# Optimization experiments

Hardware: AMD Instinct MI355X
Metric: run time of the kernel (lower is better)

## Reference

```python
import jax, jax.numpy as jnp
import numpy as np

N = 50000
E = 600000
D = 128
EPS = 1e-5  # nn.LayerNorm default eps


def gcn_conv(x, W, b, src, dst):
    # PyG GCNConv with add_self_loops=True, edge_weight=None (all ones),
    # symmetric normalization D^-1/2 (A+I) D^-1/2.
    h = x @ W                                        # [N, D]
    deg = jnp.zeros((N,), h.dtype).at[dst].add(1.0) + 1.0  # +1 for self loop
    dinv = jax.lax.rsqrt(deg)                        # deg >= 1, safe
    norm = dinv[src] * dinv[dst]                     # [E]
    msg = h[src] * norm[:, None]                     # [E, D] gather
    agg = jax.ops.segment_sum(msg, dst, num_segments=N)
    agg = agg + h * (dinv * dinv)[:, None]           # self-loop term
    return agg + b


def layer_norm(x, g, b):
    mu = jnp.mean(x, axis=-1, keepdims=True)
    var = jnp.mean(jnp.square(x - mu), axis=-1, keepdims=True)
    return (x - mu) * jax.lax.rsqrt(var + EPS) * g + b


def setup_inputs() -> dict:
    key = jax.random.key(0)
    ks = jax.random.split(key, 6)
    x = jax.random.normal(ks[0], (N, D), dtype=jnp.float32)
    edge_index = jax.random.randint(ks[1], (2, E), 0, N, dtype=jnp.int64)
    s = 1.0 / np.sqrt(D)
    W1 = jax.random.uniform(ks[2], (D, D), jnp.float32, -s, s)
    W2 = jax.random.uniform(ks[3], (D, D), jnp.float32, -s, s)
    b1 = jnp.zeros((D,), jnp.float32)
    b2 = jnp.zeros((D,), jnp.float32)
    ln1_g = jnp.ones((D,), jnp.float32)
    ln1_b = jnp.zeros((D,), jnp.float32)
    ln2_g = jnp.ones((D,), jnp.float32)
    ln2_b = jnp.zeros((D,), jnp.float32)
    return {"x": x, "edge_index": edge_index, "W1": W1, "b1": b1,
            "ln1_g": ln1_g, "ln1_b": ln1_b, "W2": W2, "b2": b2,
            "ln2_g": ln2_g, "ln2_b": ln2_b}


def reference(x, edge_index, W1, b1, ln1_g, ln1_b, W2, b2, ln2_g, ln2_b):
    src, dst = edge_index[0], edge_index[1]
    out = gcn_conv(x, W1, b1, src, dst)
    out = jax.nn.relu(layer_norm(out, ln1_g, ln1_b))  # dropout = identity (eval)
    out = gcn_conv(out, W2, b2, src, dst)
    out = jax.nn.relu(layer_norm(out, ln2_g, ln2_b))
    return out + x
```

## Files before the change

kernel.cpp:

```cpp
#include <hip/hip_runtime.h>
#include <hip/hip_fp16.h>

#define D 128
#define EPS 1e-5f

typedef unsigned int u32;
typedef unsigned short u16;
typedef __attribute__((ext_vector_type(8))) _Float16 half8;
typedef __attribute__((ext_vector_type(4))) float f32x4;

__device__ inline u16 f2h(float x) {
  _Float16 t = (_Float16)x;
  return __builtin_bit_cast(u16, t);
}
__device__ inline __half2 b2h2(u32 u) { return __builtin_bit_cast(__half2, u); }

__global__ __launch_bounds__(256) void k_prep(const float* __restrict__ W1,
                                              const float* __restrict__ W2,
                                              u16* __restrict__ Wt1,
                                              u16* __restrict__ Wt2,
                                              int* __restrict__ deg,
                                              int* __restrict__ counter, int n) {
  int i = blockIdx.x * 256 + threadIdx.x;
  if (i < n) deg[i] = 0;
  if (i == 0) *counter = 0;
  if (i < 2 * D * D) {
    const float* W = (i < D * D) ? W1 : W2;
    u16* Wt = (i < D * D) ? Wt1 : Wt2;
    int ii = i & (D * D - 1);
    int k = ii >> 7, c = ii & 127;
    Wt[c * D + k] = f2h(W[ii]);
  }
}

template <bool F32IN>
__device__ __forceinline__ void gemm_body(const void* __restrict__ in_,
                                          const u16* __restrict__ Wt,
                                          u16* __restrict__ out, int nrows,
                                          int blk) {
  const int tid = threadIdx.x;
  const int lane = tid & 63, wv = tid >> 6;
  const int m = lane & 15, q = lane >> 4;
  const int r0 = blk * 64 + wv * 16;
  const int rowa = min(r0 + m, nrows - 1);

  f32x4 acc[8];
#pragma unroll
  for (int ct = 0; ct < 8; ct++) acc[ct] = (f32x4)(0.0f);

#pragma unroll
  for (int kk = 0; kk < 4; kk++) {
    const int kbase = kk * 32 + q * 8;
    half8 a;
    if (F32IN) {
      const float* in = (const float*)in_;
      float4 v0 = *(const float4*)(in + (size_t)rowa * D + kbase);
      float4 v1 = *(const float4*)(in + (size_t)rowa * D + kbase + 4);
      a[0] = (_Float16)v0.x; a[1] = (_Float16)v0.y;
      a[2] = (_Float16)v0.z; a[3] = (_Float16)v0.w;
      a[4] = (_Float16)v1.x; a[5] = (_Float16)v1.y;
      a[6] = (_Float16)v1.z; a[7] = (_Float16)v1.w;
    } else {
      const u16* in = (const u16*)in_;
      a = *(const half8*)(in + (size_t)rowa * D + kbase);
    }
#pragma unroll
    for (int ct = 0; ct < 8; ct++) {
      half8 b = *(const half8*)(Wt + (ct * 16 + m) * D + kbase);
      acc[ct] = __builtin_amdgcn_mfma_f32_16x16x32_f16(a, b, acc[ct], 0, 0, 0);
    }
  }

#pragma unroll
  for (int ct = 0; ct < 8; ct++) {
#pragma unroll
    for (int rg = 0; rg < 4; rg++) {
      int rr = r0 + q * 4 + rg;
      if (rr < nrows) out[(size_t)rr * D + ct * 16 + m] = f2h(acc[ct][rg]);
    }
  }
}

__global__ __launch_bounds__(256) void k_deg_gemm1(
    const int* __restrict__ dst, int* __restrict__ deg, int* __restrict__ rank,
    int E, int DB,
    const float* __restrict__ x, const u16* __restrict__ Wt1,
    u16* __restrict__ A, int nrows) {
  if (blockIdx.x < (u32)DB) {
    int base = blockIdx.x * 1024 + threadIdx.x;
    int e0 = base, e1 = base + 256, e2 = base + 512, e3 = base + 768;
    int d0 = (e0 < E) ? dst[e0] : 0;
    int d1 = (e1 < E) ? dst[e1] : 0;
    int d2 = (e2 < E) ? dst[e2] : 0;
    int d3 = (e3 < E) ? dst[e3] : 0;
    int r0 = 0, r1 = 0, r2 = 0, r3 = 0;
    if (e0 < E) r0 = atomicAdd(&deg[d0], 1);
    if (e1 < E) r1 = atomicAdd(&deg[d1], 1);
    if (e2 < E) r2 = atomicAdd(&deg[d2], 1);
    if (e3 < E) r3 = atomicAdd(&deg[d3], 1);
    if (e0 < E) rank[e0] = r0;
    if (e1 < E) rank[e1] = r1;
    if (e2 < E) rank[e2] = r2;
    if (e3 < E) rank[e3] = r3;
  } else {
    gemm_body<true>(x, Wt1, A, nrows, blockIdx.x - DB);
  }
}

__global__ __launch_bounds__(256) void k_alloc(const int* __restrict__ deg,
                                               float* __restrict__ dinv,
                                               int4* __restrict__ meta,
                                               int* __restrict__ counter, int n) {
  int i = blockIdx.x * 256 + threadIdx.x;
  int lane = threadIdx.x & 63;
  int d = (i < n) ? deg[i] : 0;
  float dv = rsqrtf((float)d + 1.0f);
  int v = d;
#pragma unroll
  for (int o = 1; o < 64; o <<= 1) {
    int t = __shfl_up(v, o, 64);
    if (lane >= o) v += t;
  }
  int total = __shfl(v, 63, 64);
  int base = 0;
  if (lane == 0) base = atomicAdd(counter, total);
  base = __shfl(base, 0, 64);
  if (i < n) {
    int st = base + v - d;
    dinv[i] = dv;
    meta[i] = make_int4(st, d, __builtin_bit_cast(int, dv), 0);
  }
}

__global__ __launch_bounds__(256) void k_fill(
    const int* __restrict__ src, const int* __restrict__ dst,
    const int* __restrict__ rank, const int4* __restrict__ meta,
    const float* __restrict__ dinv, u32* __restrict__ csr, int E) {
  int base = blockIdx.x * 1024 + threadIdx.x;
#pragma unroll
  for (int t = 0; t < 4; t++) {
    int e = base + t * 256;
    if (e < E) {
      int s = src[e], d = dst[e];
      int4 mt = meta[d];
      float w = dinv[s] * __builtin_bit_cast(float, mt.z);
      csr[mt.x + rank[e]] = (u32)s | ((u32)f2h(w) << 16);
    }
  }
}

__device__ __forceinline__ void gather_ln_core(
    const uint4* __restrict__ hb, const int4* __restrict__ meta,
    const u32* __restrict__ csr, const float* __restrict__ b,
    const float* __restrict__ g, const float* __restrict__ bln,
    int row, int n, int sl, float out[8]) {
  const bool valid = row < n;
  const int rc = valid ? row : 0;
  int4 mt = meta[rc];
  int beg = mt.x;
  int cnt = valid ? mt.y : 0;
  float dv = __builtin_bit_cast(float, mt.z);
  __half2 sn2 = __float2half2_rn(dv * dv);

  uint4 su = hb[(size_t)rc * 16 + sl];
  __half2 acc0 = __hmul2(b2h2(su.x), sn2);
  __half2 acc1 = __hmul2(b2h2(su.y), sn2);
  __half2 acc2 = __hmul2(b2h2(su.z), sn2);
  __half2 acc3 = __hmul2(b2h2(su.w), sn2);

  int cm = max(cnt, __shfl_xor(cnt, 16, 64));
  cm = max(cm, __shfl_xor(cm, 32, 64));

  for (int j0 = 0; j0 < cm; j0 += 16) {
    u32 e = 0u;
    if (sl < cnt - j0) e = csr[beg + j0 + sl];
    int mm = min(cm - j0, 16);
    for (int j = 0; j < mm; j += 4) {
      u32 e0 = __shfl(e, j, 16),     e1 = __shfl(e, j + 1, 16);
      u32 e2 = __shfl(e, j + 2, 16), e3 = __shfl(e, j + 3, 16);
      uint4 v0 = hb[(size_t)(e0 & 0xffffu) * 16 + sl];
      uint4 v1 = hb[(size_t)(e1 & 0xffffu) * 16 + sl];
      uint4 v2 = hb[(size_t)(e2 & 0xffffu) * 16 + sl];
      uint4 v3 = hb[(size_t)(e3 & 0xffffu) * 16 + sl];
      __half2 w0 = b2h2((e0 >> 16) | (e0 & 0xffff0000u));
      __half2 w1 = b2h2((e1 >> 16) | (e1 & 0xffff0000u));
      __half2 w2 = b2h2((e2 >> 16) | (e2 & 0xffff0000u));
      __half2 w3 = b2h2((e3 >> 16) | (e3 & 0xffff0000u));
      acc0 = __hfma2(b2h2(v0.x), w0, acc0);
      acc1 = __hfma2(b2h2(v0.y), w0, acc1);
      acc2 = __hfma2(b2h2(v0.z), w0, acc2);
      acc3 = __hfma2(b2h2(v0.w), w0, acc3);
      acc0 = __hfma2(b2h2(v1.x), w1, acc0);
      acc1 = __hfma2(b2h2(v1.y), w1, acc1);
      acc2 = __hfma2(b2h2(v1.z), w1, acc2);
      acc3 = __hfma2(b2h2(v1.w), w1, acc3);
      acc0 = __hfma2(b2h2(v2.x), w2, acc0);
      acc1 = __hfma2(b2h2(v2.y), w2, acc1);
      acc2 = __hfma2(b2h2(v2.z), w2, acc2);
      acc3 = __hfma2(b2h2(v2.w), w2, acc3);
      acc0 = __hfma2(b2h2(v3.x), w3, acc0);
      acc1 = __hfma2(b2h2(v3.y), w3, acc1);
      acc2 = __hfma2(b2h2(v3.z), w3, acc2);
      acc3 = __hfma2(b2h2(v3.w), w3, acc3);
    }
  }

  float2 f0 = __half22float2(acc0);
  float2 f1 = __half22float2(acc1);
  float2 f2 = __half22float2(acc2);
  float2 f3 = __half22float2(acc3);
  int d0 = sl * 8;
  float4 bb0 = *(const float4*)(b + d0);
  float4 bb1 = *(const float4*)(b + d0 + 4);
  float a0 = f0.x + bb0.x, a1 = f0.y + bb0.y;
  float a2 = f1.x + bb0.z, a3 = f1.y + bb0.w;
  float a4 = f2.x + bb1.x, a5 = f2.y + bb1.y;
  float a6 = f3.x + bb1.z, a7 = f3.y + bb1.w;

  float sum = ((a0 + a1) + (a2 + a3)) + ((a4 + a5) + (a6 + a7));
#pragma unroll
  for (int o = 8; o >= 1; o >>= 1) sum += __shfl_xor(sum, o, 16);
  float mu = sum * (1.0f / 128.0f);
  float e0 = a0 - mu, e1 = a1 - mu, e2 = a2 - mu, e3 = a3 - mu;
  float e4 = a4 - mu, e5 = a5 - mu, e6 = a6 - mu, e7 = a7 - mu;
  float vs = ((e0 * e0 + e1 * e1) + (e2 * e2 + e3 * e3)) +
             ((e4 * e4 + e5 * e5) + (e6 * e6 + e7 * e7));
#pragma unroll
  for (int o = 8; o >= 1; o >>= 1) vs += __shfl_xor(vs, o, 16);
  float inv = rsqrtf(vs * (1.0f / 128.0f) + EPS);

  float4 gg0 = *(const float4*)(g + d0);
  float4 gg1 = *(const float4*)(g + d0 + 4);
  float4 bl0 = *(const float4*)(bln + d0);
  float4 bl1 = *(const float4*)(bln + d0 + 4);
  out[0] = fmaxf(e0 * inv * gg0.x + bl0.x, 0.0f);
  out[1] = fmaxf(e1 * inv * gg0.y + bl0.y, 0.0f);
  out[2] = fmaxf(e2 * inv * gg0.z + bl0.z, 0.0f);
  out[3] = fmaxf(e3 * inv * gg0.w + bl0.w, 0.0f);
  out[4] = fmaxf(e4 * inv * gg1.x + bl1.x, 0.0f);
  out[5] = fmaxf(e5 * inv * gg1.y + bl1.y, 0.0f);
  out[6] = fmaxf(e6 * inv * gg1.z + bl1.z, 0.0f);
  out[7] = fmaxf(e7 * inv * gg1.w + bl1.w, 0.0f);
}

__global__ __launch_bounds__(256) void k_mid(
    const uint4* __restrict__ hb, const int4* __restrict__ meta,
    const u32* __restrict__ csr,
    const float* __restrict__ b, const float* __restrict__ g,
    const float* __restrict__ bln,
    const u16* __restrict__ Wt2, u16* __restrict__ outB, int n) {
  __shared__ alignas(16) u16 sY[64 * 136];
  const int tid = threadIdx.x;
  const int sl = tid & 15;
  const int row0 = blockIdx.x * 64;

  for (int p = 0; p < 4; p++) {
    int lr = p * 16 + (tid >> 4);
    int row = row0 + lr;
    float o[8];
    gather_ln_core(hb, meta, csr, b, g, bln, row, n, sl, o);
    uint4 pk;
    pk.x = ((u32)f2h(o[1]) << 16) | (u32)f2h(o[0]);
    pk.y = ((u32)f2h(o[3]) << 16) | (u32)f2h(o[2]);
    pk.z = ((u32)f2h(o[5]) << 16) | (u32)f2h(o[4]);
    pk.w = ((u32)f2h(o[7]) << 16) | (u32)f2h(o[6]);
    *(uint4*)(sY + lr * 136 + sl * 8) = pk;
  }
  __syncthreads();

  const int lane = tid & 63, wv = tid >> 6;
  const int m = lane & 15, q = lane >> 4;
  f32x4 acc[8];
#pragma unroll
  for (int ct = 0; ct < 8; ct++) acc[ct] = (f32x4)(0.0f);
  const u16* ap = sY + (wv * 16 + m) * 136 + q * 8;
#pragma unroll
  for (int kk = 0; kk < 4; kk++) {
    half8 a = *(const half8*)(ap + kk * 32);
#pragma unroll
    for (int ct = 0; ct < 8; ct++) {
      half8 bfr = *(const half8*)(Wt2 + (ct * 16 + m) * D + kk * 32 + q * 8);
      acc[ct] = __builtin_amdgcn_mfma_f32_16x16x32_f16(a, bfr, acc[ct], 0, 0, 0);
    }
  }
#pragma unroll
  for (int ct = 0; ct < 8; ct++) {
#pragma unroll
    for (int rg = 0; rg < 4; rg++) {
      int rr = row0 + wv * 16 + q * 4 + rg;
      if (rr < n) outB[(size_t)rr * D + ct * 16 + m] = f2h(acc[ct][rg]);
    }
  }
}

__global__ __launch_bounds__(256) void k_gather2(
    const uint4* __restrict__ hb, const int4* __restrict__ meta,
    const u32* __restrict__ csr,
    const float* __restrict__ b, const float* __restrict__ g,
    const float* __restrict__ bln, const float* __restrict__ resid,
    float* __restrict__ outf, int n) {
  const int tid = threadIdx.x;
  const int sl = tid & 15;
  const int row = blockIdx.x * 16 + (tid >> 4);
  float o[8];
  gather_ln_core(hb, meta, csr, b, g, bln, row, n, sl, o);
  if (row >= n) return;
  size_t base = (size_t)row * D + sl * 8;
  float4 r0 = *(const float4*)(resid + base);
  float4 r1 = *(const float4*)(resid + base + 4);
  *(float4*)(outf + base) =
      make_float4(o[0] + r0.x, o[1] + r0.y, o[2] + r0.z, o[3] + r0.w);
  *(float4*)(outf + base + 4) =
      make_float4(o[4] + r1.x, o[5] + r1.y, o[6] + r1.z, o[7] + r1.w);
}

extern "C" void kernel_launch(void* const* d_in, const int* in_sizes, int n_in,
                              void* d_out, int out_size, void* d_ws, size_t ws_size,
                              hipStream_t stream) {
  const float* x    = (const float*)d_in[0];
  const int*   ei   = (const int*)d_in[1];
  const float* W1   = (const float*)d_in[2];
  const float* b1   = (const float*)d_in[3];
  const float* g1   = (const float*)d_in[4];
  const float* bl1  = (const float*)d_in[5];
  const float* W2   = (const float*)d_in[6];
  const float* b2   = (const float*)d_in[7];
  const float* g2   = (const float*)d_in[8];
  const float* bl2  = (const float*)d_in[9];

  const int N = in_sizes[0] / D;
  const int E = in_sizes[1] / 2;
  const int* src = ei;
  const int* dst = ei + E;

  size_t off = 0;
  auto walloc = [&](size_t bytes) {
    void* p = (char*)d_ws + off;
    off = (off + bytes + 255) & ~(size_t)255;
    return p;
  };
  int*   deg     = (int*)walloc((size_t)N * 4);
  float* dinv    = (float*)walloc((size_t)N * 4);
  int4*  meta    = (int4*)walloc((size_t)N * 16);
  int*   counter = (int*)walloc(256);
  int*   rank    = (int*)walloc((size_t)E * 4);
  u32*   csr     = (u32*)walloc((size_t)E * 4);
  u16*   A       = (u16*)walloc((size_t)N * D * 2);
  u16*   B       = (u16*)walloc((size_t)N * D * 2);
  u16*   Wt1     = (u16*)walloc((size_t)D * D * 2);
  u16*   Wt2     = (u16*)walloc((size_t)D * D * 2);
  float* O       = (float*)d_out;

  const int DB = (E + 1023) / 1024;
  const int FB = (E + 1023) / 1024;
  const int GB = (N + 63) / 64;

  int p0 = max(N, 2 * D * D);
  k_prep<<<(p0 + 255) / 256, 256, 0, stream>>>(W1, W2, Wt1, Wt2, deg, counter, N);
  k_deg_gemm1<<<DB + GB, 256, 0, stream>>>(dst, deg, rank, E, DB, x, Wt1, A, N);
  k_alloc<<<(N + 255) / 256, 256, 0, stream>>>(deg, dinv, meta, counter, N);
  k_fill<<<FB, 256, 0, stream>>>(src, dst, rank, meta, dinv, csr, E);
  k_mid<<<GB, 256, 0, stream>>>((const uint4*)A, meta, csr, b1, g1, bl1,
                                Wt2, B, N);
  k_gather2<<<(N + 15) / 16, 256, 0, stream>>>((const uint4*)B, meta, csr,
                                               b2, g2, bl2, x, O, N);
}
```

Measured before the change: 224.8 us.

## Build CSR via two-level bucket sort instead of global atomic degree counting

Replaces the global-atomic degree count, rank, alloc and fill pipeline with a two-level counting sort. Per-block shared-memory histograms of coarse destination buckets feed a single-block scan. The edges are then scattered into buckets, and each bucket is sorted locally in shared memory to produce CSR offsets, degrees and dinv. A separate pass fills in the edge normalization weights. The aim is to avoid contended global atomics and random scatters, at the cost of more kernel launches, a serial one-block scan, an extra temp buffer pass and only 64 blocks doing the count and scatter work.

```diff
diff --git a/kernel.cpp b/kernel.cpp
--- a/kernel.cpp
+++ b/kernel.cpp
@@ -3,6 +3,9 @@
 
 #define D 128
 #define EPS 1e-5f
+#define KB 64
+#define NBSH 7
+#define BUCKW 128
 
 typedef unsigned int u32;
 typedef unsigned short u16;
@@ -18,12 +21,8 @@
 __global__ __launch_bounds__(256) void k_prep(const float* __restrict__ W1,
                                               const float* __restrict__ W2,
                                               u16* __restrict__ Wt1,
-                                              u16* __restrict__ Wt2,
-                                              int* __restrict__ deg,
-                                              int* __restrict__ counter, int n) {
+                                              u16* __restrict__ Wt2) {
   int i = blockIdx.x * 256 + threadIdx.x;
-  if (i < n) deg[i] = 0;
-  if (i == 0) *counter = 0;
   if (i < 2 * D * D) {
     const float* W = (i < D * D) ? W1 : W2;
     u16* Wt = (i < D * D) ? Wt1 : Wt2;
@@ -81,71 +80,176 @@
   }
 }
 
-__global__ __launch_bounds__(256) void k_deg_gemm1(
-    const int* __restrict__ dst, int* __restrict__ deg, int* __restrict__ rank,
-    int E, int DB,
+__global__ __launch_bounds__(256) void k_count_gemm1(
+    const int* __restrict__ dst, int* __restrict__ cnt, int E, int NB, int EPB,
     const float* __restrict__ x, const u16* __restrict__ Wt1,
     u16* __restrict__ A, int nrows) {
-  if (blockIdx.x < (u32)DB) {
-    int base = blockIdx.x * 1024 + threadIdx.x;
-    int e0 = base, e1 = base + 256, e2 = base + 512, e3 = base + 768;
-    int d0 = (e0 < E) ? dst[e0] : 0;
-    int d1 = (e1 < E) ? dst[e1] : 0;
-    int d2 = (e2 < E) ? dst[e2] : 0;
-    int d3 = (e3 < E) ? dst[e3] : 0;
-    int r0 = 0, r1 = 0, r2 = 0, r3 = 0;
-    if (e0 < E) r0 = atomicAdd(&deg[d0], 1);
-    if (e1 < E) r1 = atomicAdd(&deg[d1], 1);
-    if (e2 < E) r2 = atomicAdd(&deg[d2], 1);
-    if (e3 < E) r3 = atomicAdd(&deg[d3], 1);
-    if (e0 < E) rank[e0] = r0;
-    if (e1 < E) rank[e1] = r1;
-    if (e2 < E) rank[e2] = r2;
-    if (e3 < E) rank[e3] = r3;
+  if (blockIdx.x < (u32)KB) {
+    __shared__ int hist[512];
+    const int k = blockIdx.x, tid = threadIdx.x;
+    for (int i = tid; i < NB; i += 256) hist[i] = 0;
+    __syncthreads();
+    const int e0 = k * EPB, e1 = min(E, e0 + EPB);
+    for (int base = e0 + tid; base < e1; base += 2048) {
+      int dd[8];
+#pragma unroll
+      for (int i = 0; i < 8; i++) {
+        int e = base + i * 256;
+        dd[i] = (e < e1) ? dst[e] : -1;
+      }
+#pragma unroll
+      for (int i = 0; i < 8; i++)
+        if (dd[i] >= 0) atomicAdd(&hist[dd[i] >> NBSH], 1);
+    }
+    __syncthreads();
+    for (int b = tid; b < NB; b += 256) cnt[b * KB + k] = hist[b];
   } else {
-    gemm_body<true>(x, Wt1, A, nrows, blockIdx.x - DB);
-  }
-}
-
-__global__ __launch_bounds__(256) void k_alloc(const int* __restrict__ deg,
-                                               float* __restrict__ dinv,
-                                               int4* __restrict__ meta,
-                                               int* __restrict__ counter, int n) {
-  int i = blockIdx.x * 256 + threadIdx.x;
-  int lane = threadIdx.x & 63;
-  int d = (i < n) ? deg[i] : 0;
-  float dv = rsqrtf((float)d + 1.0f);
-  int v = d;
-#pragma unroll
-  for (int o = 1; o < 64; o <<= 1) {
-    int t = __shfl_up(v, o, 64);
-    if (lane >= o) v += t;
-  }
-  int total = __shfl(v, 63, 64);
-  int base = 0;
-  if (lane == 0) base = atomicAdd(counter, total);
-  base = __shfl(base, 0, 64);
-  if (i < n) {
-    int st = base + v - d;
-    dinv[i] = dv;
-    meta[i] = make_int4(st, d, __builtin_bit_cast(int, dv), 0);
-  }
-}
-
-__global__ __launch_bounds__(256) void k_fill(
+    gemm_body<true>(x, Wt1, A, nrows, blockIdx.x - KB);
+  }
+}
+
+__global__ __launch_bounds__(1024) void k_scan(int* __restrict__ cnt, int M,
+                                               int NB, int* __restrict__ bsv,
+                                               int E) {
+  __shared__ int wt[16];
+  const int tid = threadIdx.x;
+  const int lane = tid & 63, wid = tid >> 6;
+  const int chunks = (M + 1023) >> 10;
+  int running = 0;
+  int i = tid;
+  int v = (i < M) ? cnt[i] : 0;
+  for (int c = 0; c < chunks; c++) {
+    int inext = i + 1024;
+    int vnext = (c + 1 < chunks && inext < M) ? cnt[inext] : 0;
+    int incl = v;
+#pragma unroll
+    for (int o = 1; o < 64; o <<= 1) {
+      int t = __shfl_up(incl, o, 64);
+      if (lane >= o) incl += t;
+    }
+    if (lane == 63) wt[wid] = incl;
+    __syncthreads();
+    int woff = 0, total = 0;
+#pragma unroll
+    for (int j = 0; j < 16; j++) {
+      int t = wt[j];
+      if (j < wid) woff += t;
+      total += t;
+    }
+    int excl = running + woff + incl - v;
+    if (i < M) {
+      cnt[i] = excl;
+      if ((i & (KB - 1)) == 0) bsv[i / KB] = excl;
+    }
+    running += total;
+    __syncthreads();
+    i = inext;
+    v = vnext;
+  }
+  if (tid == 0) bsv[NB] = E;
+}
+
+__global__ __launch_bounds__(256) void k_scatter(
     const int* __restrict__ src, const int* __restrict__ dst,
-    const int* __restrict__ rank, const int4* __restrict__ meta,
-    const float* __restrict__ dinv, u32* __restrict__ csr, int E) {
-  int base = blockIdx.x * 1024 + threadIdx.x;
-#pragma unroll
-  for (int t = 0; t < 4; t++) {
-    int e = base + t * 256;
-    if (e < E) {
-      int s = src[e], d = dst[e];
-      int4 mt = meta[d];
-      float w = dinv[s] * __builtin_bit_cast(float, mt.z);
-      csr[mt.x + rank[e]] = (u32)s | ((u32)f2h(w) << 16);
-    }
+    const int* __restrict__ cnt, u32* __restrict__ tmp, int E, int NB,
+    int EPB) {
+  __shared__ int off[512];
+  const int k = blockIdx.x, tid = threadIdx.x;
+  for (int b = tid; b < NB; b += 256) off[b] = cnt[b * KB + k];
+  __syncthreads();
+  const int e0 = k * EPB, e1 = min(E, e0 + EPB);
+  for (int base = e0 + tid; base < e1; base += 2048) {
+    int dd[8], ss[8];
+#pragma unroll
+    for (int i = 0; i < 8; i++) {
+      int e = base + i * 256;
+      dd[i] = (e < e1) ? dst[e] : -1;
+      ss[i] = (e < e1) ? src[e] : 0;
+    }
+#pragma unroll
+    for (int i = 0; i < 8; i++) {
+      if (dd[i] >= 0) {
+        int p = atomicAdd(&off[dd[i] >> NBSH], 1);
+        tmp[p] = (u32)ss[i] | ((u32)(dd[i] & (BUCKW - 1)) << 16);
+      }
+    }
+  }
+}
+
+__global__ __launch_bounds__(256) void k_bucket(
+    const u32* __restrict__ tmp, const int* __restrict__ bsv,
+    int4* __restrict__ meta, float* __restrict__ dinv,
+    u32* __restrict__ csr, int N) {
+  __shared__ int hist[BUCKW];
+  __shared__ int sc[BUCKW];
+  __shared__ int cur[BUCKW];
+  const int b = blockIdx.x, tid = threadIdx.x;
+  const int s0 = bsv[b], s1 = bsv[b + 1];
+  if (tid < BUCKW) hist[tid] = 0;
+  __syncthreads();
+  for (int base = s0 + tid; base < s1; base += 1024) {
+    int tt[4];
+#pragma unroll
+    for (int i = 0; i < 4; i++) {
+      int idx = base + i * 256;
+      tt[i] = (idx < s1) ? (int)tmp[idx] : -1;
+    }
+#pragma unroll
+    for (int i = 0; i < 4; i++)
+      if (tt[i] >= 0) atomicAdd(&hist[(tt[i] >> 16) & (BUCKW - 1)], 1);
+  }
+  __syncthreads();
+  if (tid < BUCKW) sc[tid] = hist[tid];
+  __syncthreads();
+#pragma unroll
+  for (int o = 1; o < BUCKW; o <<= 1) {
+    int t = 0;
+    if (tid < BUCKW && tid >= o) t = sc[tid - o];
+    __syncthreads();
+    if (tid < BUCKW) sc[tid] += t;
+    __syncthreads();
+  }
+  if (tid < BUCKW) {
+    int dg = hist[tid];
+    int excl = sc[tid] - dg;
+    cur[tid] = excl;
+    int d = (b << NBSH) + tid;
+    if (d < N) {
+      float dv = rsqrtf((float)dg + 1.0f);
+      meta[d] = make_int4(s0 + excl, dg, __builtin_bit_cast(int, dv), 0);
+      dinv[d] = dv;
+    }
+  }
+  __syncthreads();
+  for (int base = s0 + tid; base < s1; base += 1024) {
+    int tt[4];
+#pragma unroll
+    for (int i = 0; i < 4; i++) {
+      int idx = base + i * 256;
+      tt[i] = (idx < s1) ? (int)tmp[idx] : -1;
+    }
+#pragma unroll
+    for (int i = 0; i < 4; i++) {
+      if (tt[i] >= 0) {
+        int r = atomicAdd(&cur[(tt[i] >> 16) & (BUCKW - 1)], 1);
+        csr[s0 + r] = (u32)tt[i] & 0xffffu;
+      }
+    }
+  }
+}
+
+__global__ __launch_bounds__(256) void k_weights(
+    const int4* __restrict__ meta, const float* __restrict__ dinv,
+    u32* __restrict__ csr, int N) {
+  int gid = blockIdx.x * 256 + threadIdx.x;
+  int r = gid >> 2, j0 = gid & 3;
+  if (r >= N) return;
+  int4 mt = meta[r];
+  float dv = __builtin_bit_cast(float, mt.z);
+  for (int j = j0; j < mt.y; j += 4) {
+    u32 s = csr[mt.x + j];
+    float w = dinv[s] * dv;
+    csr[mt.x + j] = s | ((u32)f2h(w) << 16);
   }
 }
 
@@ -333,33 +437,35 @@
   const int* src = ei;
   const int* dst = ei + E;
 
+  const int NB  = (N + BUCKW - 1) / BUCKW;
+  const int M   = NB * KB;
+  const int EPB = (E + KB - 1) / KB;
+  const int GB  = (N + 63) / 64;
+
   size_t off = 0;
   auto walloc = [&](size_t bytes) {
     void* p = (char*)d_ws + off;
     off = (off + bytes + 255) & ~(size_t)255;
     return p;
   };
-  int*   deg     = (int*)walloc((size_t)N * 4);
-  float* dinv    = (float*)walloc((size_t)N * 4);
-  int4*  meta    = (int4*)walloc((size_t)N * 16);
-  int*   counter = (int*)walloc(256);
-  int*   rank    = (int*)walloc((size_t)E * 4);
-  u32*   csr     = (u32*)walloc((size_t)E * 4);
-  u16*   A       = (u16*)walloc((size_t)N * D * 2);
-  u16*   B       = (u16*)walloc((size_t)N * D * 2);
-  u16*   Wt1     = (u16*)walloc((size_t)D * D * 2);
-  u16*   Wt2     = (u16*)walloc((size_t)D * D * 2);
-  float* O       = (float*)d_out;
-
-  const int DB = (E + 1023) / 1024;
-  const int FB = (E + 1023) / 1024;
-  const int GB = (N + 63) / 64;
-
-  int p0 = max(N, 2 * D * D);
-  k_prep<<<(p0 + 255) / 256, 256, 0, stream>>>(W1, W2, Wt1, Wt2, deg, counter, N);
-  k_deg_gemm1<<<DB + GB, 256, 0, stream>>>(dst, deg, rank, E, DB, x, Wt1, A, N);
-  k_alloc<<<(N + 255) / 256, 256, 0, stream>>>(deg, dinv, meta, counter, N);
-  k_fill<<<FB, 256, 0, stream>>>(src, dst, rank, meta, dinv, csr, E);
+  int*   cnt   = (int*)walloc((size_t)M * 4);
+  int*   bsv   = (int*)walloc((size_t)(NB + 1) * 4);
+  u32*   tmp   = (u32*)walloc((size_t)E * 4);
+  u32*   csr   = (u32*)walloc((size_t)E * 4);
+  int4*  meta  = (int4*)walloc((size_t)N * 16);
+  float* dinv  = (float*)walloc((size_t)N * 4);
+  u16*   A     = (u16*)walloc((size_t)N * D * 2);
+  u16*   B     = (u16*)walloc((size_t)N * D * 2);
+  u16*   Wt1   = (u16*)walloc((size_t)D * D * 2);
+  u16*   Wt2   = (u16*)walloc((size_t)D * D * 2);
+  float* O     = (float*)d_out;
+
+  k_prep<<<(2 * D * D + 255) / 256, 256, 0, stream>>>(W1, W2, Wt1, Wt2);
+  k_count_gemm1<<<KB + GB, 256, 0, stream>>>(dst, cnt, E, NB, EPB, x, Wt1, A, N);
+  k_scan<<<1, 1024, 0, stream>>>(cnt, M, NB, bsv, E);
+  k_scatter<<<KB, 256, 0, stream>>>(src, dst, cnt, tmp, E, NB, EPB);
+  k_bucket<<<NB, 256, 0, stream>>>(tmp, bsv, meta, dinv, csr, N);
+  k_weights<<<(N * 4 + 255) / 256, 256, 0, stream>>>(meta, dinv, csr, N);
   k_mid<<<GB, 256, 0, stream>>>((const uint4*)A, meta, csr, b1, g1, bl1,
                                 Wt2, B, N);
   k_gather2<<<(N + 15) / 16, 256, 0, stream>>>((const uint4*)B, meta, csr,
```

Result: faster. 217.9 us (-3.1%).
